# Kernel tuning notes

Measured on AMD Instinct MI355X. Metric: run time of the kernel, lower is better.

## Reference

```python
import jax, jax.numpy as jnp
import numpy as np

N, E = 40000, 640000
DIN, C, EDIM = 128, 128, 32  # heads=1, out_channels=128

def setup_inputs() -> dict:
    key = jax.random.key(0)
    ks = jax.random.split(key, 9)
    x = jax.random.normal(ks[0], (N, DIN), dtype=jnp.float32)
    edge_index = jax.random.randint(ks[1], (2, E), 0, N, dtype=jnp.int64)
    edge_attr = jax.random.normal(ks[2], (E, EDIM), dtype=jnp.float32)
    s = 1.0 / np.sqrt(DIN)
    W = jax.random.normal(ks[3], (DIN, C), dtype=jnp.float32) * s
    W_edge = jax.random.normal(ks[4], (EDIM, C), dtype=jnp.float32) / np.sqrt(EDIM)
    att_src = jax.random.normal(ks[5], (C,), dtype=jnp.float32) * s
    att_dst = jax.random.normal(ks[6], (C,), dtype=jnp.float32) * s
    att_edge = jax.random.normal(ks[7], (C,), dtype=jnp.float32) * s
    bias = jnp.zeros((C,), dtype=jnp.float32)
    return {"x": x, "edge_index": edge_index, "edge_attr": edge_attr,
            "W": W, "W_edge": W_edge, "att_src": att_src, "att_dst": att_dst,
            "att_edge": att_edge, "bias": bias}

def reference(x, edge_index, edge_attr, W, W_edge, att_src, att_dst, att_edge, bias):
    # GATConv (heads=1) with edge features
    h = x @ W                      # [N, C] transformed node features
    a_src = h @ att_src            # [N] per-node source attention logits
    a_dst = h @ att_dst            # [N]
    src, dst = edge_index[0], edge_index[1]
    e = edge_attr @ W_edge         # [E, C]
    a_edge = e @ att_edge          # [E]
    alpha = a_src[src] + a_dst[dst] + a_edge            # [E]
    alpha = jax.nn.leaky_relu(alpha, negative_slope=0.2)
    # segment softmax over incoming edges of each destination node
    amax = jax.ops.segment_max(alpha, dst, num_segments=N)
    amax = jnp.where(jnp.isfinite(amax), amax, 0.0)     # empty segments -> -inf guard
    ex = jnp.exp(alpha - amax[dst])
    denom = jax.ops.segment_sum(ex, dst, num_segments=N)
    w = ex / (denom[dst] + 1e-16)                       # PyG softmax epsilon
    out = jax.ops.segment_sum(h[src] * w[:, None], dst, num_segments=N)  # [N, C]
    return out + bias
```

## Files before the change

### kernel.cpp

```cpp
#include <hip/hip_runtime.h>
#include <hip/hip_bf16.h>
#include <hip/hip_fp16.h>


#define DIN 128
#define CCH 128
#define EDIM 32
#define XS_LD 68

__device__ __forceinline__ unsigned pack_bf2(float a, float b) {
    __hip_bfloat16 x = __float2bfloat16(a);
    __hip_bfloat16 y = __float2bfloat16(b);
    unsigned short ux = *(unsigned short*)&x;
    unsigned short uy = *(unsigned short*)&y;
    return (unsigned)ux | ((unsigned)uy << 16);
}

__global__ __launch_bounds__(256) void gemm_h(
    const float* __restrict__ x, const float* __restrict__ W,
    const float* __restrict__ att_src, const float* __restrict__ att_dst,
    const int* __restrict__ ei, unsigned* __restrict__ hb,
    float* __restrict__ a_src, float* __restrict__ a_dst,
    int* __restrict__ count, unsigned short* __restrict__ rank,
    int N, int E) {
    __shared__ float xs[64 * XS_LD];
    __shared__ float wl[64 * CCH];
    const int t = threadIdx.x;
    const int tx = t & 15;
    const int ty = t >> 4;
    const int row0 = blockIdx.x * 64;

    {
        const int* eid = ei + E;
        const int stride = gridDim.x * 256;
        for (int e = blockIdx.x * 256 + t; e < E; e += stride) {
            int r = atomicAdd(&count[eid[e]], 1);
            rank[e] = (unsigned short)r;
        }
    }

    float acc[4][8];
#pragma unroll
    for (int r = 0; r < 4; ++r)
#pragma unroll
        for (int c = 0; c < 8; ++c) acc[r][c] = 0.0f;

    for (int kh = 0; kh < 2; ++kh) {
        __syncthreads();
        {
            const float4* xg = (const float4*)x;
#pragma unroll
            for (int i = 0; i < 4; ++i) {
                int j4 = t + 256 * i;
                int r = j4 >> 4;
                int k = (j4 & 15) * 4;
                float4 v = xg[(size_t)(row0 + r) * 32 + kh * 16 + (j4 & 15)];
                *(float4*)&xs[r * XS_LD + k] = v;
            }
        }
        {
            const float4* wg = (const float4*)W;
#pragma unroll
            for (int i = 0; i < 8; ++i) {
                int j4 = t + 256 * i;
                int k = j4 >> 5;
                int c4 = j4 & 31;
                float4 v = wg[(size_t)(kh * 64 + k) * 32 + c4];
                *(float4*)&wl[k * CCH + c4 * 4] = v;
            }
        }
        __syncthreads();

#pragma unroll 4
        for (int k4 = 0; k4 < 64; k4 += 4) {
            float xr[4][4];
#pragma unroll
            for (int r = 0; r < 4; ++r) {
                float4 v = *(const float4*)&xs[(ty * 4 + r) * XS_LD + k4];
                xr[r][0] = v.x; xr[r][1] = v.y; xr[r][2] = v.z; xr[r][3] = v.w;
            }
            float wr[4][8];
#pragma unroll
            for (int i = 0; i < 4; ++i) {
                float4 w0 = *(const float4*)&wl[(k4 + i) * CCH + tx * 8];
                float4 w1 = *(const float4*)&wl[(k4 + i) * CCH + tx * 8 + 4];
                wr[i][0] = w0.x; wr[i][1] = w0.y; wr[i][2] = w0.z; wr[i][3] = w0.w;
                wr[i][4] = w1.x; wr[i][5] = w1.y; wr[i][6] = w1.z; wr[i][7] = w1.w;
            }
#pragma unroll
            for (int i = 0; i < 4; ++i)
#pragma unroll
                for (int r = 0; r < 4; ++r)
#pragma unroll
                    for (int c = 0; c < 8; ++c)
                        acc[r][c] += xr[r][i] * wr[i][c];
        }
    }

    float asv[8], adv[8];
#pragma unroll
    for (int c = 0; c < 8; ++c) {
        asv[c] = att_src[tx * 8 + c];
        adv[c] = att_dst[tx * 8 + c];
    }
#pragma unroll
    for (int r = 0; r < 4; ++r) {
        const int row = row0 + ty * 4 + r;
        unsigned u0 = pack_bf2(acc[r][0], acc[r][1]);
        unsigned u1 = pack_bf2(acc[r][2], acc[r][3]);
        unsigned u2 = pack_bf2(acc[r][4], acc[r][5]);
        unsigned u3 = pack_bf2(acc[r][6], acc[r][7]);
        *(uint4*)&hb[(size_t)row * 64 + tx * 4] = make_uint4(u0, u1, u2, u3);
        float ps = 0.0f, pd = 0.0f;
#pragma unroll
        for (int c = 0; c < 8; ++c) {
            ps += acc[r][c] * asv[c];
            pd += acc[r][c] * adv[c];
        }
        ps += __shfl_down(ps, 8, 16);
        pd += __shfl_down(pd, 8, 16);
        ps += __shfl_down(ps, 4, 16);
        pd += __shfl_down(pd, 4, 16);
        ps += __shfl_down(ps, 2, 16);
        pd += __shfl_down(pd, 2, 16);
        ps += __shfl_down(ps, 1, 16);
        pd += __shfl_down(pd, 1, 16);
        if (tx == 0) {
            a_src[row] = ps;
            a_dst[row] = pd;
        }
    }
}

__global__ __launch_bounds__(256) void scan_part(const int* __restrict__ count,
                                                 int* __restrict__ bsum, int N4) {
    int i4 = blockIdx.x * 256 + threadIdx.x;
    int s = 0;
    if (i4 < N4) {
        int4 vv = ((const int4*)count)[i4];
        s = vv.x + vv.y + vv.z + vv.w;
    }
#pragma unroll
    for (int off = 32; off; off >>= 1) s += __shfl_down(s, off);
    __shared__ int wsum[4];
    if ((threadIdx.x & 63) == 0) wsum[threadIdx.x >> 6] = s;
    __syncthreads();
    if (threadIdx.x == 0)
        bsum[blockIdx.x] = wsum[0] + wsum[1] + wsum[2] + wsum[3];
}

__global__ __launch_bounds__(256) void scan_apply(
    const int* __restrict__ count, const int* __restrict__ bsum,
    const float* __restrict__ a_dst, int* __restrict__ offs,
    float2* __restrict__ dinfo, int N4) {
    __shared__ int s_boff;
    __shared__ int wt[4];
    if (threadIdx.x == 0) {
        int s = 0;
        for (int i = 0; i < (int)blockIdx.x; ++i) s += bsum[i];
        s_boff = s;
    }
    int i4 = blockIdx.x * 256 + threadIdx.x;
    int4 vv = make_int4(0, 0, 0, 0);
    if (i4 < N4) vv = ((const int4*)count)[i4];
    int s = vv.x + vv.y + vv.z + vv.w;
    int lane = threadIdx.x & 63, w = threadIdx.x >> 6;
    int inc = s;
#pragma unroll
    for (int off = 1; off < 64; off <<= 1) {
        int u = __shfl_up(inc, off);
        if (lane >= off) inc += u;
    }
    if (lane == 63) wt[w] = inc;
    __syncthreads();
    int woff = 0;
    for (int i = 0; i < w; ++i) woff += wt[i];
    int exd = s_boff + woff + inc - s;
    if (i4 < N4) {
        int4 o;
        o.x = exd;
        o.y = exd + vv.x;
        o.z = exd + vv.x + vv.y;
        o.w = exd + vv.x + vv.y + vv.z;
        ((int4*)offs)[i4] = o;
        float4 ad = ((const float4*)a_dst)[i4];
        float4 d0 = make_float4(ad.x, __int_as_float(o.x),
                                ad.y, __int_as_float(o.y));
        float4 d1 = make_float4(ad.z, __int_as_float(o.z),
                                ad.w, __int_as_float(o.w));
        ((float4*)dinfo)[i4 * 2] = d0;
        ((float4*)dinfo)[i4 * 2 + 1] = d1;
    }
}

__global__ __launch_bounds__(256) void edge_fill(
    const int* __restrict__ ei, const float* __restrict__ ea,
    const float* __restrict__ W_edge, const float* __restrict__ att_edge,
    const float* __restrict__ a_src, const float2* __restrict__ dinfo,
    const unsigned short* __restrict__ rank, unsigned* __restrict__ pairs,
    int E) {
    __shared__ float vpart[8][EDIM];
    __shared__ float vl[EDIM];
    const int t = threadIdx.x;
    {
        int j = t & 31, seg = t >> 5;
        const float* wr = W_edge + j * CCH + seg * 16;
        const float* ar = att_edge + seg * 16;
        float p = 0.0f;
#pragma unroll
        for (int k = 0; k < 16; ++k) p += wr[k] * ar[k];
        vpart[seg][j] = p;
    }
    __syncthreads();
    if (t < EDIM) {
        float s = 0.0f;
#pragma unroll
        for (int i = 0; i < 8; ++i) s += vpart[i][t];
        vl[t] = s;
    }
    __syncthreads();

    const int base = blockIdx.x * 1024 + t;
    int eidx[4], sn[4], dn[4], rk[4];
    bool ok[4];
#pragma unroll
    for (int i = 0; i < 4; ++i) {
        eidx[i] = base + 256 * i;
        ok[i] = eidx[i] < E;
    }
#pragma unroll
    for (int i = 0; i < 4; ++i) {
        sn[i] = ok[i] ? ei[eidx[i]] : 0;
        dn[i] = ok[i] ? ei[E + eidx[i]] : 0;
    }
#pragma unroll
    for (int i = 0; i < 4; ++i) rk[i] = ok[i] ? (int)rank[eidx[i]] : 0;
    float asv[4];
    float2 di[4];
#pragma unroll
    for (int i = 0; i < 4; ++i) {
        asv[i] = a_src[sn[i]];
        di[i] = dinfo[dn[i]];
    }
    float dot[4];
#pragma unroll
    for (int i = 0; i < 4; ++i) {
        float s = 0.0f;
        if (ok[i]) {
            const float4* ea4 = (const float4*)(ea + (size_t)eidx[i] * EDIM);
#pragma unroll
            for (int j = 0; j < 8; ++j) {
                float4 q = ea4[j];
                s += q.x * vl[4 * j] + q.y * vl[4 * j + 1] +
                     q.z * vl[4 * j + 2] + q.w * vl[4 * j + 3];
            }
        }
        dot[i] = s;
    }
#pragma unroll
    for (int i = 0; i < 4; ++i) {
        if (!ok[i]) continue;
        float alpha = asv[i] + di[i].x + dot[i];
        alpha = alpha > 0.0f ? alpha : 0.2f * alpha;
        float ex = __expf(alpha);
        unsigned rec = (unsigned)(unsigned short)sn[i] |
                       ((unsigned)__half_as_ushort(__float2half(ex)) << 16);
        int p = __float_as_int(di[i].y) + rk[i];
        pairs[p] = rec;
    }
}

#define GATHER_EDGE(rec)                                                      \
    {                                                                         \
        unsigned q = hb[(size_t)((rec) & 0xffffu) * 64 + lane];               \
        float exv = __half2float(__ushort_as_half((unsigned short)((rec) >> 16))); \
        a0 += exv * __uint_as_float(q << 16);                                 \
        a1 += exv * __uint_as_float(q & 0xffff0000u);                         \
        sum += exv;                                                           \
    }

__global__ __launch_bounds__(256) void gather_k(
    const int* __restrict__ count, const int* __restrict__ offs,
    const unsigned* __restrict__ pairs, const unsigned* __restrict__ hb,
    const float* __restrict__ bias, float* __restrict__ out, int N) {
    int n = blockIdx.x * 4 + (threadIdx.x >> 6);
    int lane = threadIdx.x & 63;
    if (n >= N) return;
    int cnt = count[n];
    int start = offs[n];
    float a0 = 0.0f, a1 = 0.0f, sum = 0.0f;
    int j = 0;
    int head = (4 - (start & 3)) & 3;
    if (head > cnt) head = cnt;
    for (; j < head; ++j) {
        unsigned r = pairs[start + j];
        GATHER_EDGE(r);
    }
    int nq = (cnt - j) >> 2;
    if (nq > 0) {
        const uint4* pp4 = (const uint4*)(pairs + start + j);
        uint4 cur = pp4[0];
        for (int g = 0; g + 1 < nq; ++g) {
            uint4 nxt = pp4[g + 1];
            unsigned q0 = hb[(size_t)(cur.x & 0xffffu) * 64 + lane];
            unsigned q1 = hb[(size_t)(cur.y & 0xffffu) * 64 + lane];
            unsigned q2 = hb[(size_t)(cur.z & 0xffffu) * 64 + lane];
            unsigned q3 = hb[(size_t)(cur.w & 0xffffu) * 64 + lane];
            float e0 = __half2float(__ushort_as_half((unsigned short)(cur.x >> 16)));
            float e1 = __half2float(__ushort_as_half((unsigned short)(cur.y >> 16)));
            float e2 = __half2float(__ushort_as_half((unsigned short)(cur.z >> 16)));
            float e3 = __half2float(__ushort_as_half((unsigned short)(cur.w >> 16)));
            a0 += e0 * __uint_as_float(q0 << 16);
            a1 += e0 * __uint_as_float(q0 & 0xffff0000u);
            a0 += e1 * __uint_as_float(q1 << 16);
            a1 += e1 * __uint_as_float(q1 & 0xffff0000u);
            a0 += e2 * __uint_as_float(q2 << 16);
            a1 += e2 * __uint_as_float(q2 & 0xffff0000u);
            a0 += e3 * __uint_as_float(q3 << 16);
            a1 += e3 * __uint_as_float(q3 & 0xffff0000u);
            sum += (e0 + e1) + (e2 + e3);
            cur = nxt;
        }
        {
            unsigned q0 = hb[(size_t)(cur.x & 0xffffu) * 64 + lane];
            unsigned q1 = hb[(size_t)(cur.y & 0xffffu) * 64 + lane];
            unsigned q2 = hb[(size_t)(cur.z & 0xffffu) * 64 + lane];
            unsigned q3 = hb[(size_t)(cur.w & 0xffffu) * 64 + lane];
            float e0 = __half2float(__ushort_as_half((unsigned short)(cur.x >> 16)));
            float e1 = __half2float(__ushort_as_half((unsigned short)(cur.y >> 16)));
            float e2 = __half2float(__ushort_as_half((unsigned short)(cur.z >> 16)));
            float e3 = __half2float(__ushort_as_half((unsigned short)(cur.w >> 16)));
            a0 += e0 * __uint_as_float(q0 << 16);
            a1 += e0 * __uint_as_float(q0 & 0xffff0000u);
            a0 += e1 * __uint_as_float(q1 << 16);
            a1 += e1 * __uint_as_float(q1 & 0xffff0000u);
            a0 += e2 * __uint_as_float(q2 << 16);
            a1 += e2 * __uint_as_float(q2 & 0xffff0000u);
            a0 += e3 * __uint_as_float(q3 << 16);
            a1 += e3 * __uint_as_float(q3 & 0xffff0000u);
            sum += (e0 + e1) + (e2 + e3);
        }
        j += nq * 4;
    }
    for (; j < cnt; ++j) {
        unsigned r = pairs[start + j];
        GATHER_EDGE(r);
    }
    float inv = 1.0f / (sum + 1e-16f);
    float2 bv = *(const float2*)&bias[2 * lane];
    float2 o;
    o.x = a0 * inv + bv.x;
    o.y = a1 * inv + bv.y;
    *(float2*)&out[(size_t)n * CCH + 2 * lane] = o;
}

extern "C" void kernel_launch(void* const* d_in, const int* in_sizes, int n_in,
                              void* d_out, int out_size, void* d_ws, size_t ws_size,
                              hipStream_t stream) {
    const float* x        = (const float*)d_in[0];
    const int*   ei       = (const int*)d_in[1];
    const float* ea       = (const float*)d_in[2];
    const float* W        = (const float*)d_in[3];
    const float* W_edge   = (const float*)d_in[4];
    const float* att_src  = (const float*)d_in[5];
    const float* att_dst  = (const float*)d_in[6];
    const float* att_edge = (const float*)d_in[7];
    const float* bias     = (const float*)d_in[8];
    float* out = (float*)d_out;

    const int N = in_sizes[0] / DIN;
    const int E = in_sizes[2] / EDIM;
    const int N4 = N / 4;
    const int NB = (N4 + 255) / 256;

    char* ws = (char*)d_ws;
    unsigned*       hb    = (unsigned*)ws;
    unsigned*       pairs = (unsigned*)(ws + (size_t)N * 64 * 4);
    unsigned short* rank  = (unsigned short*)(pairs + E);
    float*  a_src = (float*)((char*)rank + (size_t)E * 2);
    float*  a_dst = a_src + N;
    float2* dinfo = (float2*)(a_dst + N);
    int*    count = (int*)(dinfo + N);
    int*    offs  = count + N;
    int*    bsum  = offs + N;

    hipMemsetAsync(count, 0, (size_t)N * sizeof(int), stream);

    gemm_h<<<N / 64, 256, 0, stream>>>(x, W, att_src, att_dst, ei, hb,
                                       a_src, a_dst, count, rank, N, E);
    scan_part<<<NB, 256, 0, stream>>>(count, bsum, N4);
    scan_apply<<<NB, 256, 0, stream>>>(count, bsum, a_dst, offs, dinfo, N4);
    edge_fill<<<(E + 1023) / 1024, 256, 0, stream>>>(ei, ea, W_edge, att_edge,
                                                     a_src, dinfo, rank, pairs, E);
    gather_k<<<(N + 3) / 4, 256, 0, stream>>>(count, offs, pairs, hb, bias, out, N);
}
```

Baseline: 256.9 us.

## Use split-bf16 MFMA for node GEMM and fuse edge-logit dot into it

Replaces the scalar FP32 node GEMM with bf16 MFMA instructions, splitting each operand into high and low bf16 halves and doing three MFMAs to keep near-FP32 accuracy. Moves the edge_attr·(W_edge·att_edge) dot product out of edge_fill into gemm_h, stored as an fp16 value packed with the rank into a 32-bit erec word. edge_fill then reads one word per edge instead of 128 bytes of edge_attr. The costs are extra conversion work while staging tiles, fp16 rounding of the edge logit, and the 16-bit rank and logit writes landing in the same word from separate stores.

```diff
diff --git a/kernel.cpp b/kernel.cpp
--- a/kernel.cpp
+++ b/kernel.cpp
@@ -6,28 +6,42 @@
 #define DIN 128
 #define CCH 128
 #define EDIM 32
-#define XS_LD 68
-
+#define LDK 40
+
+typedef __attribute__((ext_vector_type(8))) short short8v;
+typedef __attribute__((ext_vector_type(4))) float f32x4;
+
+__device__ __forceinline__ unsigned short f2b(float v) {
+    __hip_bfloat16 b = __float2bfloat16(v);
+    return *(unsigned short*)&b;
+}
+__device__ __forceinline__ float b2f(unsigned short u) {
+    return __uint_as_float((unsigned)u << 16);
+}
 __device__ __forceinline__ unsigned pack_bf2(float a, float b) {
-    __hip_bfloat16 x = __float2bfloat16(a);
-    __hip_bfloat16 y = __float2bfloat16(b);
-    unsigned short ux = *(unsigned short*)&x;
-    unsigned short uy = *(unsigned short*)&y;
-    return (unsigned)ux | ((unsigned)uy << 16);
-}
-
-__global__ __launch_bounds__(256) void gemm_h(
+    return (unsigned)f2b(a) | ((unsigned)f2b(b) << 16);
+}
+
+__global__ __launch_bounds__(256, 4) void gemm_h(
     const float* __restrict__ x, const float* __restrict__ W,
     const float* __restrict__ att_src, const float* __restrict__ att_dst,
-    const int* __restrict__ ei, unsigned* __restrict__ hb,
-    float* __restrict__ a_src, float* __restrict__ a_dst,
-    int* __restrict__ count, unsigned short* __restrict__ rank,
-    int N, int E) {
-    __shared__ float xs[64 * XS_LD];
-    __shared__ float wl[64 * CCH];
+    const float* __restrict__ W_edge, const float* __restrict__ att_edge,
+    const int* __restrict__ ei, const float* __restrict__ ea,
+    unsigned* __restrict__ hb, float* __restrict__ a_src,
+    float* __restrict__ a_dst, unsigned* __restrict__ erec,
+    int* __restrict__ count, int N, int E) {
+    __shared__ unsigned short xs_h[64 * LDK];
+    __shared__ unsigned short xs_l[64 * LDK];
+    __shared__ unsigned short wt_h[128 * LDK];
+    __shared__ unsigned short wt_l[128 * LDK];
+    __shared__ float vpart[8][EDIM];
+    __shared__ float vl[EDIM];
+
     const int t = threadIdx.x;
-    const int tx = t & 15;
-    const int ty = t >> 4;
+    const int ln = t & 63;
+    const int wv = t >> 6;
+    const int lr = ln & 15;
+    const int lk = ln >> 4;
     const int row0 = blockIdx.x * 64;
 
     {
@@ -35,99 +49,142 @@
         const int stride = gridDim.x * 256;
         for (int e = blockIdx.x * 256 + t; e < E; e += stride) {
             int r = atomicAdd(&count[eid[e]], 1);
-            rank[e] = (unsigned short)r;
-        }
-    }
-
-    float acc[4][8];
-#pragma unroll
-    for (int r = 0; r < 4; ++r)
-#pragma unroll
-        for (int c = 0; c < 8; ++c) acc[r][c] = 0.0f;
-
-    for (int kh = 0; kh < 2; ++kh) {
+            ((unsigned short*)&erec[e])[0] = (unsigned short)r;
+        }
+    }
+
+    {
+        int j = t & 31, seg = t >> 5;
+        const float* wr = W_edge + j * CCH + seg * 16;
+        const float* ar = att_edge + seg * 16;
+        float p = 0.0f;
+#pragma unroll
+        for (int k = 0; k < 16; ++k) p += wr[k] * ar[k];
+        vpart[seg][j] = p;
+    }
+    __syncthreads();
+    if (t < EDIM) {
+        float s = 0.0f;
+#pragma unroll
+        for (int i = 0; i < 8; ++i) s += vpart[i][t];
+        vl[t] = s;
+    }
+
+    f32x4 acc[8];
+#pragma unroll
+    for (int cf = 0; cf < 8; ++cf) acc[cf] = (f32x4)(0.0f);
+
+    const float4* x4 = (const float4*)x;
+    const float4* W4 = (const float4*)W;
+
+    for (int q = 0; q < 4; ++q) {
         __syncthreads();
+#pragma unroll
+        for (int i = 0; i < 2; ++i) {
+            int j4 = t + 256 * i;
+            int r = j4 >> 3;
+            int f4 = j4 & 7;
+            float4 v = x4[(size_t)(row0 + r) * 32 + q * 8 + f4];
+            float vv[4] = {v.x, v.y, v.z, v.w};
+            unsigned short h[4], l[4];
+#pragma unroll
+            for (int m = 0; m < 4; ++m) {
+                h[m] = f2b(vv[m]);
+                l[m] = f2b(vv[m] - b2f(h[m]));
+            }
+            uint2 uh = make_uint2((unsigned)h[0] | ((unsigned)h[1] << 16),
+                                  (unsigned)h[2] | ((unsigned)h[3] << 16));
+            uint2 ul = make_uint2((unsigned)l[0] | ((unsigned)l[1] << 16),
+                                  (unsigned)l[2] | ((unsigned)l[3] << 16));
+            *(uint2*)&xs_h[r * LDK + f4 * 4] = uh;
+            *(uint2*)&xs_l[r * LDK + f4 * 4] = ul;
+        }
         {
-            const float4* xg = (const float4*)x;
+            int kt = t >> 5;
+            int ct = t & 31;
+            float w4[4][4];
 #pragma unroll
             for (int i = 0; i < 4; ++i) {
-                int j4 = t + 256 * i;
-                int r = j4 >> 4;
-                int k = (j4 & 15) * 4;
-                float4 v = xg[(size_t)(row0 + r) * 32 + kh * 16 + (j4 & 15)];
-                *(float4*)&xs[r * XS_LD + k] = v;
+                float4 v = W4[(size_t)(q * 32 + kt * 4 + i) * 32 + ct];
+                w4[i][0] = v.x; w4[i][1] = v.y; w4[i][2] = v.z; w4[i][3] = v.w;
             }
-        }
-        {
-            const float4* wg = (const float4*)W;
-#pragma unroll
-            for (int i = 0; i < 8; ++i) {
-                int j4 = t + 256 * i;
-                int k = j4 >> 5;
-                int c4 = j4 & 31;
-                float4 v = wg[(size_t)(kh * 64 + k) * 32 + c4];
-                *(float4*)&wl[k * CCH + c4 * 4] = v;
+#pragma unroll
+            for (int cc = 0; cc < 4; ++cc) {
+                unsigned short h[4], l[4];
+#pragma unroll
+                for (int i = 0; i < 4; ++i) {
+                    h[i] = f2b(w4[i][cc]);
+                    l[i] = f2b(w4[i][cc] - b2f(h[i]));
+                }
+                uint2 uh = make_uint2((unsigned)h[0] | ((unsigned)h[1] << 16),
+                                      (unsigned)h[2] | ((unsigned)h[3] << 16));
+                uint2 ul = make_uint2((unsigned)l[0] | ((unsigned)l[1] << 16),
+                                      (unsigned)l[2] | ((unsigned)l[3] << 16));
+                int c = ct * 4 + cc;
+                *(uint2*)&wt_h[c * LDK + kt * 4] = uh;
+                *(uint2*)&wt_l[c * LDK + kt * 4] = ul;
             }
         }
         __syncthreads();
 
-#pragma unroll 4
-        for (int k4 = 0; k4 < 64; k4 += 4) {
-            float xr[4][4];
-#pragma unroll
-            for (int r = 0; r < 4; ++r) {
-                float4 v = *(const float4*)&xs[(ty * 4 + r) * XS_LD + k4];
-                xr[r][0] = v.x; xr[r][1] = v.y; xr[r][2] = v.z; xr[r][3] = v.w;
+        short8v bh = *(const short8v*)&xs_h[(wv * 16 + lr) * LDK + lk * 8];
+        short8v bl = *(const short8v*)&xs_l[(wv * 16 + lr) * LDK + lk * 8];
+#pragma unroll
+        for (int cf = 0; cf < 8; ++cf) {
+            short8v ah = *(const short8v*)&wt_h[(cf * 16 + lr) * LDK + lk * 8];
+            short8v al = *(const short8v*)&wt_l[(cf * 16 + lr) * LDK + lk * 8];
+            acc[cf] = __builtin_amdgcn_mfma_f32_16x16x32_bf16(ah, bh, acc[cf], 0, 0, 0);
+            acc[cf] = __builtin_amdgcn_mfma_f32_16x16x32_bf16(ah, bl, acc[cf], 0, 0, 0);
+            acc[cf] = __builtin_amdgcn_mfma_f32_16x16x32_bf16(al, bh, acc[cf], 0, 0, 0);
+        }
+    }
+
+    {
+        const int row = row0 + wv * 16 + lr;
+        float ps = 0.0f, pd = 0.0f;
+#pragma unroll
+        for (int cf = 0; cf < 8; ++cf) {
+            int c0 = cf * 16 + lk * 4;
+            float4 as4 = *(const float4*)&att_src[c0];
+            float4 ad4 = *(const float4*)&att_dst[c0];
+            ps += acc[cf][0] * as4.x + acc[cf][1] * as4.y +
+                  acc[cf][2] * as4.z + acc[cf][3] * as4.w;
+            pd += acc[cf][0] * ad4.x + acc[cf][1] * ad4.y +
+                  acc[cf][2] * ad4.z + acc[cf][3] * ad4.w;
+            uint2 u = make_uint2(pack_bf2(acc[cf][0], acc[cf][1]),
+                                 pack_bf2(acc[cf][2], acc[cf][3]));
+            *(uint2*)&hb[(size_t)row * 64 + cf * 8 + lk * 2] = u;
+        }
+        ps += __shfl_xor(ps, 16);
+        ps += __shfl_xor(ps, 32);
+        pd += __shfl_xor(pd, 16);
+        pd += __shfl_xor(pd, 32);
+        if (ln < 16) {
+            a_src[row0 + wv * 16 + ln] = ps;
+            a_dst[row0 + wv * 16 + ln] = pd;
+        }
+    }
+
+    {
+        float vlr[EDIM];
+#pragma unroll
+        for (int j = 0; j < EDIM; ++j) vlr[j] = vl[j];
+        const float4* ea4 = (const float4*)ea;
+        const int e0 = blockIdx.x * 1024 + t;
+#pragma unroll
+        for (int i = 0; i < 4; ++i) {
+            int e = e0 + 256 * i;
+            if (e < E) {
+                float s = 0.0f;
+#pragma unroll
+                for (int j = 0; j < 8; ++j) {
+                    float4 v = ea4[(size_t)e * 8 + j];
+                    s += v.x * vlr[4 * j] + v.y * vlr[4 * j + 1] +
+                         v.z * vlr[4 * j + 2] + v.w * vlr[4 * j + 3];
+                }
+                ((unsigned short*)&erec[e])[1] =
+                    __half_as_ushort(__float2half(s));
             }
-            float wr[4][8];
-#pragma unroll
-            for (int i = 0; i < 4; ++i) {
-                float4 w0 = *(const float4*)&wl[(k4 + i) * CCH + tx * 8];
-                float4 w1 = *(const float4*)&wl[(k4 + i) * CCH + tx * 8 + 4];
-                wr[i][0] = w0.x; wr[i][1] = w0.y; wr[i][2] = w0.z; wr[i][3] = w0.w;
-                wr[i][4] = w1.x; wr[i][5] = w1.y; wr[i][6] = w1.z; wr[i][7] = w1.w;
-            }
-#pragma unroll
-            for (int i = 0; i < 4; ++i)
-#pragma unroll
-                for (int r = 0; r < 4; ++r)
-#pragma unroll
-                    for (int c = 0; c < 8; ++c)
-                        acc[r][c] += xr[r][i] * wr[i][c];
-        }
-    }
-
-    float asv[8], adv[8];
-#pragma unroll
-    for (int c = 0; c < 8; ++c) {
-        asv[c] = att_src[tx * 8 + c];
-        adv[c] = att_dst[tx * 8 + c];
-    }
-#pragma unroll
-    for (int r = 0; r < 4; ++r) {
-        const int row = row0 + ty * 4 + r;
-        unsigned u0 = pack_bf2(acc[r][0], acc[r][1]);
-        unsigned u1 = pack_bf2(acc[r][2], acc[r][3]);
-        unsigned u2 = pack_bf2(acc[r][4], acc[r][5]);
-        unsigned u3 = pack_bf2(acc[r][6], acc[r][7]);
-        *(uint4*)&hb[(size_t)row * 64 + tx * 4] = make_uint4(u0, u1, u2, u3);
-        float ps = 0.0f, pd = 0.0f;
-#pragma unroll
-        for (int c = 0; c < 8; ++c) {
-            ps += acc[r][c] * asv[c];
-            pd += acc[r][c] * adv[c];
-        }
-        ps += __shfl_down(ps, 8, 16);
-        pd += __shfl_down(pd, 8, 16);
-        ps += __shfl_down(ps, 4, 16);
-        pd += __shfl_down(pd, 4, 16);
-        ps += __shfl_down(ps, 2, 16);
-        pd += __shfl_down(pd, 2, 16);
-        ps += __shfl_down(ps, 1, 16);
-        pd += __shfl_down(pd, 1, 16);
-        if (tx == 0) {
-            a_src[row] = ps;
-            a_dst[row] = pd;
         }
     }
 }
@@ -194,34 +251,13 @@
 }
 
 __global__ __launch_bounds__(256) void edge_fill(
-    const int* __restrict__ ei, const float* __restrict__ ea,
-    const float* __restrict__ W_edge, const float* __restrict__ att_edge,
+    const int* __restrict__ ei, const unsigned* __restrict__ erec,
     const float* __restrict__ a_src, const float2* __restrict__ dinfo,
-    const unsigned short* __restrict__ rank, unsigned* __restrict__ pairs,
-    int E) {
-    __shared__ float vpart[8][EDIM];
-    __shared__ float vl[EDIM];
+    unsigned* __restrict__ pairs, int E) {
     const int t = threadIdx.x;
-    {
-        int j = t & 31, seg = t >> 5;
-        const float* wr = W_edge + j * CCH + seg * 16;
-        const float* ar = att_edge + seg * 16;
-        float p = 0.0f;
-#pragma unroll
-        for (int k = 0; k < 16; ++k) p += wr[k] * ar[k];
-        vpart[seg][j] = p;
-    }
-    __syncthreads();
-    if (t < EDIM) {
-        float s = 0.0f;
-#pragma unroll
-        for (int i = 0; i < 8; ++i) s += vpart[i][t];
-        vl[t] = s;
-    }
-    __syncthreads();
-
     const int base = blockIdx.x * 1024 + t;
     int eidx[4], sn[4], dn[4], rk[4];
+    float ae[4];
     bool ok[4];
 #pragma unroll
     for (int i = 0; i < 4; ++i) {
@@ -234,7 +270,11 @@
         dn[i] = ok[i] ? ei[E + eidx[i]] : 0;
     }
 #pragma unroll
-    for (int i = 0; i < 4; ++i) rk[i] = ok[i] ? (int)rank[eidx[i]] : 0;
+    for (int i = 0; i < 4; ++i) {
+        unsigned er = ok[i] ? erec[eidx[i]] : 0u;
+        rk[i] = (int)(er & 0xffffu);
+        ae[i] = __half2float(__ushort_as_half((unsigned short)(er >> 16)));
+    }
     float asv[4];
     float2 di[4];
 #pragma unroll
@@ -242,25 +282,10 @@
         asv[i] = a_src[sn[i]];
         di[i] = dinfo[dn[i]];
     }
-    float dot[4];
-#pragma unroll
-    for (int i = 0; i < 4; ++i) {
-        float s = 0.0f;
-        if (ok[i]) {
-            const float4* ea4 = (const float4*)(ea + (size_t)eidx[i] * EDIM);
-#pragma unroll
-            for (int j = 0; j < 8; ++j) {
-                float4 q = ea4[j];
-                s += q.x * vl[4 * j] + q.y * vl[4 * j + 1] +
-                     q.z * vl[4 * j + 2] + q.w * vl[4 * j + 3];
-            }
-        }
-        dot[i] = s;
-    }
 #pragma unroll
     for (int i = 0; i < 4; ++i) {
         if (!ok[i]) continue;
-        float alpha = asv[i] + di[i].x + dot[i];
+        float alpha = asv[i] + di[i].x + ae[i];
         alpha = alpha > 0.0f ? alpha : 0.2f * alpha;
         float ex = __expf(alpha);
         unsigned rec = (unsigned)(unsigned short)sn[i] |
@@ -374,10 +399,10 @@
     const int NB = (N4 + 255) / 256;
 
     char* ws = (char*)d_ws;
-    unsigned*       hb    = (unsigned*)ws;
-    unsigned*       pairs = (unsigned*)(ws + (size_t)N * 64 * 4);
-    unsigned short* rank  = (unsigned short*)(pairs + E);
-    float*  a_src = (float*)((char*)rank + (size_t)E * 2);
+    unsigned* hb    = (unsigned*)ws;
+    unsigned* pairs = (unsigned*)(ws + (size_t)N * 64 * 4);
+    unsigned* erec  = pairs + E;
+    float*  a_src = (float*)(erec + E);
     float*  a_dst = a_src + N;
     float2* dinfo = (float2*)(a_dst + N);
     int*    count = (int*)(dinfo + N);
@@ -386,11 +411,12 @@
 
     hipMemsetAsync(count, 0, (size_t)N * sizeof(int), stream);
 
-    gemm_h<<<N / 64, 256, 0, stream>>>(x, W, att_src, att_dst, ei, hb,
-                                       a_src, a_dst, count, rank, N, E);
+    gemm_h<<<N / 64, 256, 0, stream>>>(x, W, att_src, att_dst, W_edge, att_edge,
+                                       ei, ea, hb, a_src, a_dst, erec,
+                                       count, N, E);
     scan_part<<<NB, 256, 0, stream>>>(count, bsum, N4);
     scan_apply<<<NB, 256, 0, stream>>>(count, bsum, a_dst, offs, dinfo, N4);
-    edge_fill<<<(E + 1023) / 1024, 256, 0, stream>>>(ei, ea, W_edge, att_edge,
-                                                     a_src, dinfo, rank, pairs, E);
+    edge_fill<<<(E + 1023) / 1024, 256, 0, stream>>>(ei, erec, a_src, dinfo,
+                                                     pairs, E);
     gather_k<<<(N + 3) / 4, 256, 0, stream>>>(count, offs, pairs, hb, bias, out, N);
 }
```

Measured after the change: 238.9 us. 7.0% less time.
